# Optimization experiments

Hardware: AMD Instinct MI355X
Metric: run time of the kernel (lower is better)

## Reference

```python
import jax, jax.numpy as jnp
import numpy as np

E = 512
M = 65536


def setup_inputs() -> dict:
    key = jax.random.key(0)
    ks = jax.random.split(key, 10)
    return {
        "x": jax.random.uniform(ks[0], (M, 5), dtype=jnp.float32),
        "w_bet": jax.random.normal(ks[1], (E,), dtype=jnp.float32),
        "b_bet": jax.random.normal(ks[2], (E,), dtype=jnp.float32),
        "w_stack": jax.random.normal(ks[3], (E,), dtype=jnp.float32),
        "b_stack": jax.random.normal(ks[4], (E,), dtype=jnp.float32),
        "w_call": jax.random.normal(ks[5], (E,), dtype=jnp.float32),
        "b_call": jax.random.normal(ks[6], (E,), dtype=jnp.float32),
        "w_odds": jax.random.normal(ks[7], (E,), dtype=jnp.float32),
        "b_odds": jax.random.normal(ks[8], (E,), dtype=jnp.float32),
        "order_table": jax.random.normal(ks[9], (5, E), dtype=jnp.float32),
    }


def reference(x, w_bet, b_bet, w_stack, b_stack, w_call, b_call, w_odds, b_odds, order_table):
    # Linear(1,E)(s) == s * w + b  (w is the [E,1] weight squeezed).
    # stack_fc is shared between hero (col 1) and villain (col 2).
    m = x.shape[0]
    bet = x[:, 0:1] * w_bet + (b_bet + order_table[0])        # [M, E]
    hero = x[:, 1:2] * w_stack + (b_stack + order_table[1])
    villain = x[:, 2:3] * w_stack + (b_stack + order_table[2])
    call = x[:, 3:4] * w_call + (b_call + order_table[3])
    odd = x[:, 4:5] * w_odds + (b_odds + order_table[4])
    # torch.stack(..., dim=-1).view(M, -1): interleaved [M, E, 5] -> [M, 5E]
    out = jnp.stack((bet, hero, villain, call, odd), axis=-1).reshape(m, -1)
    return out
```

## Files before the change

kernel.cpp:

```cpp
#include <hip/hip_runtime.h>


#define ROWS_PER_IT 2
#define ITERS 16

__global__ __launch_bounds__(256) void pc_kernel(
    const float* __restrict__ x,
    const float* __restrict__ w_bet,  const float* __restrict__ b_bet,
    const float* __restrict__ w_stk,  const float* __restrict__ b_stk,
    const float* __restrict__ w_call, const float* __restrict__ b_call,
    const float* __restrict__ w_odds, const float* __restrict__ b_odds,
    const float* __restrict__ ot,
    float* __restrict__ out)
{
    __shared__ float4 stage[1280];
    const int tid  = threadIdx.x;
    const int t0   = tid & 127;
    const int half = tid >> 7;

    const float* wsrc[5] = {w_bet, w_stk, w_stk, w_call, w_odds};
    const float* bsrc[5] = {b_bet, b_stk, b_stk, b_call, b_odds};
    float wv[5][4], bv[5][4];
#pragma unroll
    for (int c = 0; c < 5; ++c) {
        float4 w4 = reinterpret_cast<const float4*>(wsrc[c])[t0];
        float4 b4 = reinterpret_cast<const float4*>(bsrc[c])[t0];
        float4 o4 = reinterpret_cast<const float4*>(ot + 512 * c)[t0];
        wv[c][0] = w4.x; wv[c][1] = w4.y; wv[c][2] = w4.z; wv[c][3] = w4.w;
        bv[c][0] = b4.x + o4.x; bv[c][1] = b4.y + o4.y;
        bv[c][2] = b4.z + o4.z; bv[c][3] = b4.w + o4.w;
    }

    const long long rp_base = (long long)blockIdx.x * ITERS;

    for (int it = 0; it < ITERS; ++it) {
        const long long rp = rp_base + it;
        const int m = (int)(2 * rp) + half;

        const float* xr = x + m * 5;
        float xs[5];
#pragma unroll
        for (int c = 0; c < 5; ++c) xs[c] = xr[c];

        float v[4][5];
#pragma unroll
        for (int j = 0; j < 4; ++j)
#pragma unroll
            for (int c = 0; c < 5; ++c)
                v[j][c] = fmaf(xs[c], wv[c][j], bv[c][j]);

        float4* st = stage + half * 640 + t0 * 5;
#pragma unroll
        for (int q = 0; q < 5; ++q) {
            float4 f;
            f.x = v[(4 * q + 0) / 5][(4 * q + 0) % 5];
            f.y = v[(4 * q + 1) / 5][(4 * q + 1) % 5];
            f.z = v[(4 * q + 2) / 5][(4 * q + 2) % 5];
            f.w = v[(4 * q + 3) / 5][(4 * q + 3) % 5];
            st[q] = f;
        }
        __syncthreads();

        float4* dst = reinterpret_cast<float4*>(out) + rp * 1280;
#pragma unroll
        for (int k = 0; k < 5; ++k)
            dst[tid + 256 * k] = stage[tid + 256 * k];
        __syncthreads();
    }
}

extern "C" void kernel_launch(void* const* d_in, const int* in_sizes, int n_in,
                              void* d_out, int out_size, void* d_ws, size_t ws_size,
                              hipStream_t stream) {
    const float* x      = (const float*)d_in[0];
    const float* w_bet  = (const float*)d_in[1];
    const float* b_bet  = (const float*)d_in[2];
    const float* w_stk  = (const float*)d_in[3];
    const float* b_stk  = (const float*)d_in[4];
    const float* w_call = (const float*)d_in[5];
    const float* b_call = (const float*)d_in[6];
    const float* w_odds = (const float*)d_in[7];
    const float* b_odds = (const float*)d_in[8];
    const float* ot     = (const float*)d_in[9];
    float* out = (float*)d_out;

    const int M = in_sizes[0] / 5;
    const int grid = M / (ROWS_PER_IT * ITERS);

    pc_kernel<<<grid, 256, 0, stream>>>(x, w_bet, b_bet, w_stk, b_stk,
                                        w_call, b_call, w_odds, b_odds, ot, out);
}
```

Before: 136.0 us.

## Precompute per-thread interleaved weights to write output directly without LDS staging

Each thread now owns four fixed interleaved output positions of a row. It builds the matching weight, bias and column index once through a shared-memory table, then writes one float4 per row straight to global memory. This removes the per-row LDS staging and the two barriers per iteration. The cost is a 640-thread block, gathered x loads indexed by column, and 32 rows per block.

```diff
diff --git a/kernel.cpp b/kernel.cpp
--- a/kernel.cpp
+++ b/kernel.cpp
@@ -1,10 +1,10 @@
 #include <hip/hip_runtime.h>
 
 
-#define ROWS_PER_IT 2
-#define ITERS 16
+#define ROWS_PER_BLOCK 32
+#define THREADS 640
 
-__global__ __launch_bounds__(256) void pc_kernel(
+__global__ __launch_bounds__(THREADS) void pc_kernel(
     const float* __restrict__ x,
     const float* __restrict__ w_bet,  const float* __restrict__ b_bet,
     const float* __restrict__ w_stk,  const float* __restrict__ b_stk,
@@ -13,59 +13,56 @@
     const float* __restrict__ ot,
     float* __restrict__ out)
 {
-    __shared__ float4 stage[1280];
-    const int tid  = threadIdx.x;
-    const int t0   = tid & 127;
-    const int half = tid >> 7;
+    __shared__ float tw[2560];
+    __shared__ float tb[2560];
 
-    const float* wsrc[5] = {w_bet, w_stk, w_stk, w_call, w_odds};
-    const float* bsrc[5] = {b_bet, b_stk, b_stk, b_call, b_odds};
-    float wv[5][4], bv[5][4];
+    const int tid = threadIdx.x;
+
+    {
+        const int c  = tid >> 7;
+        const int e0 = (tid & 127) * 4;
+        const float* wp; const float* bp;
+        if      (c == 0) { wp = w_bet;  bp = b_bet;  }
+        else if (c == 1) { wp = w_stk;  bp = b_stk;  }
+        else if (c == 2) { wp = w_stk;  bp = b_stk;  }
+        else if (c == 3) { wp = w_call; bp = b_call; }
+        else             { wp = w_odds; bp = b_odds; }
+        float4 w4 = *reinterpret_cast<const float4*>(wp + e0);
+        float4 b4 = *reinterpret_cast<const float4*>(bp + e0);
+        float4 o4 = *reinterpret_cast<const float4*>(ot + c * 512 + e0);
+        *reinterpret_cast<float4*>(tw + c * 512 + e0) = w4;
+        float4 bb;
+        bb.x = b4.x + o4.x; bb.y = b4.y + o4.y;
+        bb.z = b4.z + o4.z; bb.w = b4.w + o4.w;
+        *reinterpret_cast<float4*>(tb + c * 512 + e0) = bb;
+    }
+    __syncthreads();
+
+    float wv[4], bv[4];
+    int   cj[4];
 #pragma unroll
-    for (int c = 0; c < 5; ++c) {
-        float4 w4 = reinterpret_cast<const float4*>(wsrc[c])[t0];
-        float4 b4 = reinterpret_cast<const float4*>(bsrc[c])[t0];
-        float4 o4 = reinterpret_cast<const float4*>(ot + 512 * c)[t0];
-        wv[c][0] = w4.x; wv[c][1] = w4.y; wv[c][2] = w4.z; wv[c][3] = w4.w;
-        bv[c][0] = b4.x + o4.x; bv[c][1] = b4.y + o4.y;
-        bv[c][2] = b4.z + o4.z; bv[c][3] = b4.w + o4.w;
+    for (int j = 0; j < 4; ++j) {
+        int w = 4 * tid + j;
+        int e = w / 5;
+        int c = w - 5 * e;
+        cj[j] = c;
+        wv[j] = tw[c * 512 + e];
+        bv[j] = tb[c * 512 + e];
     }
 
-    const long long rp_base = (long long)blockIdx.x * ITERS;
+    const int m_base = blockIdx.x * ROWS_PER_BLOCK;
+    float4* outv = reinterpret_cast<float4*>(out);
 
-    for (int it = 0; it < ITERS; ++it) {
-        const long long rp = rp_base + it;
-        const int m = (int)(2 * rp) + half;
-
+#pragma unroll 4
+    for (int r = 0; r < ROWS_PER_BLOCK; ++r) {
+        const int m = m_base + r;
         const float* xr = x + m * 5;
-        float xs[5];
-#pragma unroll
-        for (int c = 0; c < 5; ++c) xs[c] = xr[c];
-
-        float v[4][5];
-#pragma unroll
-        for (int j = 0; j < 4; ++j)
-#pragma unroll
-            for (int c = 0; c < 5; ++c)
-                v[j][c] = fmaf(xs[c], wv[c][j], bv[c][j]);
-
-        float4* st = stage + half * 640 + t0 * 5;
-#pragma unroll
-        for (int q = 0; q < 5; ++q) {
-            float4 f;
-            f.x = v[(4 * q + 0) / 5][(4 * q + 0) % 5];
-            f.y = v[(4 * q + 1) / 5][(4 * q + 1) % 5];
-            f.z = v[(4 * q + 2) / 5][(4 * q + 2) % 5];
-            f.w = v[(4 * q + 3) / 5][(4 * q + 3) % 5];
-            st[q] = f;
-        }
-        __syncthreads();
-
-        float4* dst = reinterpret_cast<float4*>(out) + rp * 1280;
-#pragma unroll
-        for (int k = 0; k < 5; ++k)
-            dst[tid + 256 * k] = stage[tid + 256 * k];
-        __syncthreads();
+        float4 v;
+        v.x = fmaf(xr[cj[0]], wv[0], bv[0]);
+        v.y = fmaf(xr[cj[1]], wv[1], bv[1]);
+        v.z = fmaf(xr[cj[2]], wv[2], bv[2]);
+        v.w = fmaf(xr[cj[3]], wv[3], bv[3]);
+        outv[(size_t)m * 640 + tid] = v;
     }
 }
 
@@ -84,9 +81,10 @@
     const float* ot     = (const float*)d_in[9];
     float* out = (float*)d_out;
 
-    const int M = in_sizes[0] / 5;
-    const int grid = M / (ROWS_PER_IT * ITERS);
+    const int M    = in_sizes[0] / 5;
+    const int grid = M / ROWS_PER_BLOCK;
 
-    pc_kernel<<<grid, 256, 0, stream>>>(x, w_bet, b_bet, w_stk, b_stk,
-                                        w_call, b_call, w_odds, b_odds, ot, out);
+    pc_kernel<<<grid, THREADS, 0, stream>>>(x, w_bet, b_bet, w_stk, b_stk,
+                                            w_call, b_call, w_odds, b_odds,
+                                            ot, out);
 }
```

Result: slower. 242.0 us (+78.0%).
